# Kernel tuning notes

Hardware: AMD Instinct MI355X
Metric: run time of the kernel (lower is better)

The kernel has to match this reference:

```python
import jax, jax.numpy as jnp
import numpy as np

B, C, H, W = 4, 256, 64, 64
EPS = 1e-6


def setup_inputs() -> dict:
    key = jax.random.key(0)
    ks = jax.random.split(key, 6)
    x = jax.random.normal(ks[0], (B, C, H, W), jnp.float32)
    gn_w = jnp.ones((1, C, 1, 1), jnp.float32)
    gn_b = jnp.zeros((1, C, 1, 1), jnp.float32)
    s = 1.0 / np.sqrt(C)
    w0 = jax.random.normal(ks[1], (C, C), jnp.float32) * s
    w1 = jax.random.normal(ks[2], (C, C), jnp.float32) * s
    w2 = jax.random.normal(ks[3], (C, C), jnp.float32) * s
    w3 = jax.random.normal(ks[4], (C, C), jnp.float32) * s
    b0 = jnp.zeros((C,), jnp.float32)
    b1 = jnp.zeros((C,), jnp.float32)
    b2 = jnp.zeros((C,), jnp.float32)
    b3 = jnp.zeros((C,), jnp.float32)
    return {"x": x, "gn_w": gn_w, "gn_b": gn_b,
            "w0": w0, "b0": b0, "w1": w1, "b1": b1,
            "w2": w2, "b2": b2, "w3": w3, "b3": b3}


def _nin(t, Wm, bv):
    # 1x1 conv as channel matmul: (B,C,H,W) x (C,D) -> (B,D,H,W)
    return jnp.einsum('bchw,cd->bdhw', t, Wm) + bv[None, :, None, None]


def reference(x, gn_w, gn_b, w0, b0, w1, b1, w2, b2, w3, b3):
    Bb, Cc, Hh, Ww = x.shape
    G = min(Cc // 4, 32)  # GroupLayerNorm2d groups
    # per-pixel group norm: normalize over channels within each group only
    xg = x.reshape(Bb, G, Cc // G, Hh, Ww)
    mean = xg.mean(axis=2, keepdims=True)
    var = xg.var(axis=2, keepdims=True)
    hn = ((xg - mean) / jnp.sqrt(var + EPS)).reshape(Bb, Cc, Hh, Ww)
    hn = hn * gn_w + gn_b
    q = _nin(hn, w0, b0)
    k = _nin(hn, w1, b1)
    v = _nin(hn, w2, b2)
    # full (B,H,W,H,W) scores; mask is causal along W only (key col j > query col w)
    scores = jnp.einsum('bchw,bcij->bhwij', q, k) * (float(Cc) ** -0.5)
    causal = jnp.triu(jnp.ones((Ww, Ww), bool), k=1)  # (W_query, W_key)
    scores = jnp.where(causal[None, None, :, None, :], -jnp.inf, scores)
    attn = jax.nn.softmax(scores.reshape(Bb, Hh, Ww, Hh * Ww), axis=-1)
    attn = attn.reshape(Bb, Hh, Ww, Hh, Ww)
    h = jnp.einsum('bhwij,bcij->bchw', attn, v)
    return x + _nin(h, w3, b3)  # skip_rescale=False
```

## Files before the change

### kernel.cpp

```cpp
#include <hip/hip_runtime.h>
#include <math.h>

#define LOG2E 1.4426950408889634f

typedef __attribute__((ext_vector_type(8))) __bf16 bf16x8_t;
typedef __attribute__((ext_vector_type(8))) short short8_t;
typedef __attribute__((ext_vector_type(4))) short short4_t;
typedef __attribute__((ext_vector_type(4))) float f32x4;

static __device__ __forceinline__ short f2bf(float f){
    unsigned u = __builtin_bit_cast(unsigned, f);
    unsigned r = (u + 0x7fffu + ((u >> 16) & 1u)) >> 16;
    return (short)r;
}
static __device__ __forceinline__ float bf2f(short s){
    return __builtin_bit_cast(float, (unsigned)((unsigned short)s) << 16);
}

static __device__ __forceinline__ f32x4 mfma16(short8_t a, short8_t b, f32x4 c){
    return __builtin_amdgcn_mfma_f32_16x16x32_bf16(
        __builtin_bit_cast(bf16x8_t, a), __builtin_bit_cast(bf16x8_t, b), c, 0, 0, 0);
}

static __device__ __forceinline__ float swz16(float v){
    return __builtin_bit_cast(float,
        __builtin_amdgcn_ds_swizzle(__builtin_bit_cast(int, v), 0x401F));
}
static __device__ __forceinline__ float bperm32(int addr, float v){
    return __builtin_bit_cast(float,
        __builtin_amdgcn_ds_bpermute(addr, __builtin_bit_cast(int, v)));
}

static __device__ __forceinline__ void gload_lds16(const void* g, void* l){
    __builtin_amdgcn_global_load_lds(
        (const __attribute__((address_space(1))) unsigned char*)g,
        (__attribute__((address_space(3))) unsigned char*)l, 16, 0, 0);
}

__global__ __launch_bounds__(256) void prep_w(const float* __restrict__ w0,
    const float* __restrict__ w1, const float* __restrict__ w2,
    const float* __restrict__ w3, short* __restrict__ wT)
{
    __shared__ float T[64 * 65];
    const int mat = blockIdx.x >> 4, tile = blockIdx.x & 15;
    const int c0 = (tile >> 2) * 64, d0 = (tile & 3) * 64;
    const float* src = mat == 0 ? w0 : mat == 1 ? w1 : mat == 2 ? w2 : w3;
    const int t = threadIdx.x;
    #pragma unroll
    for (int i = 0; i < 4; i++){
        int r = (t >> 4) + i * 16, c4 = (t & 15) * 4;
        f32x4 v = *(const f32x4*)(src + (size_t)(c0 + r) * 256 + d0 + c4);
        #pragma unroll
        for (int j = 0; j < 4; j++) T[r * 65 + c4 + j] = v[j];
    }
    __syncthreads();
    int drow = t >> 2, cb = (t & 3) * 16;
    short tmp[16];
    #pragma unroll
    for (int j = 0; j < 16; j++) tmp[j] = f2bf(T[(cb + j) * 65 + drow]);
    short* dst = wT + (size_t)mat * 65536 + (size_t)(d0 + drow) * 256 + c0 + cb;
    *(short8_t*)dst = *(short8_t*)tmp;
    *(short8_t*)(dst + 8) = *(short8_t*)(tmp + 8);
}

__global__ __launch_bounds__(256) void gn_kernel(const float* __restrict__ x,
    const float* __restrict__ gnw, const float* __restrict__ gnb,
    short* __restrict__ hn)
{
    int flat = blockIdx.x * 256 + threadIdx.x;
    int n = flat & 4095, g = (flat >> 12) & 31, b = flat >> 17;
    const float* xp = x + (size_t)(b * 256 + g * 8) * 4096 + n;
    float v[8], s = 0.f, s2 = 0.f;
    #pragma unroll
    for (int k = 0; k < 8; k++){ float t = xp[(size_t)k * 4096]; v[k] = t; s += t; s2 += t * t; }
    float mean = s * 0.125f;
    float var  = s2 * 0.125f - mean * mean;
    float inv  = rsqrtf(var + 1e-6f);
    int h = n >> 6, w = n & 63, m = w * 64 + h;
    short o[8];
    #pragma unroll
    for (int k = 0; k < 8; k++)
        o[k] = f2bf((v[k] - mean) * inv * gnw[g * 8 + k] + gnb[g * 8 + k]);
    *(short8_t*)(hn + (size_t)(b * 4096 + m) * 256 + g * 8) = *(short8_t*)o;
}

__global__ __launch_bounds__(256) void qkv_gemm(const short* __restrict__ hn,
    const short* __restrict__ wT, const float* __restrict__ bq,
    const float* __restrict__ bk, const float* __restrict__ bv,
    short* __restrict__ Q, short* __restrict__ Kf, short* __restrict__ Vf)
{
    __shared__ short As[64 * 72];
    __shared__ short Bs[64 * 72];
    __shared__ float CT[64 * 65];

    const int tid = threadIdx.x;
    const int m0 = blockIdx.x * 64;
    const int by = blockIdx.y;
    const int mat = by >> 2;
    const int d0 = (by & 3) * 64;
    const short* w = wT + mat * 65536;
    const float* bias = mat == 0 ? bq : mat == 1 ? bk : bv;

    const int wv = tid >> 6, lane = tid & 63;
    const int wrow = (wv >> 1) * 32, wcol = (wv & 1) * 32;
    const int lrow = lane & 15, lq = lane >> 4;

    f32x4 acc[2][2] = {};

    for (int k0 = 0; k0 < 256; k0 += 64){
        __syncthreads();
        #pragma unroll
        for (int i = 0; i < 2; i++){
            int idx = tid + i * 256, r = idx >> 3, c = (idx & 7) * 8;
            *(short8_t*)&As[r * 72 + c] = *(const short8_t*)(hn + (size_t)(m0 + r) * 256 + k0 + c);
            *(short8_t*)&Bs[r * 72 + c] = *(const short8_t*)(w  + (size_t)(d0 + r) * 256 + k0 + c);
        }
        __syncthreads();
        #pragma unroll
        for (int kk = 0; kk < 2; kk++){
            int off = kk * 32 + lq * 8;
            short8_t a0  = *(short8_t*)&As[(wrow + lrow) * 72 + off];
            short8_t a1  = *(short8_t*)&As[(wrow + 16 + lrow) * 72 + off];
            short8_t b0v = *(short8_t*)&Bs[(wcol + lrow) * 72 + off];
            short8_t b1v = *(short8_t*)&Bs[(wcol + 16 + lrow) * 72 + off];
            acc[0][0] = mfma16(a0, b0v, acc[0][0]);
            acc[0][1] = mfma16(a0, b1v, acc[0][1]);
            acc[1][0] = mfma16(a1, b0v, acc[1][0]);
            acc[1][1] = mfma16(a1, b1v, acc[1][1]);
        }
    }

    const int b = m0 >> 12, kb64 = (m0 & 4095) >> 6;

    if (mat == 0){
        #pragma unroll
        for (int i = 0; i < 2; i++)
          #pragma unroll
          for (int j = 0; j < 2; j++)
            #pragma unroll
            for (int r = 0; r < 4; r++){
                int row = wrow + i * 16 + lq * 4 + r;
                int col = wcol + j * 16 + lrow;
                Q[(size_t)(m0 + row) * 256 + d0 + col] = f2bf((acc[i][j][r] + bias[d0 + col]) * 0.0625f);
            }
    } else if (mat == 1){
        #pragma unroll
        for (int i = 0; i < 2; i++)
          #pragma unroll
          for (int j = 0; j < 2; j++)
            #pragma unroll
            for (int r = 0; r < 4; r++){
                int row = wrow + i * 16 + lq * 4 + r;
                int col = wcol + j * 16 + lrow;
                CT[row * 65 + col] = acc[i][j][r] + bias[d0 + col];
            }
        __syncthreads();
        int key = tid >> 2, c16 = (tid & 3) * 16;
        int kc = key >> 4, l15 = key & 15;
        #pragma unroll
        for (int half = 0; half < 2; half++){
            int ch0 = c16 + half * 8;
            int ks = (d0 + ch0) >> 5, lqf = (ch0 & 31) >> 3;
            short tmp[8];
            #pragma unroll
            for (int j = 0; j < 8; j++) tmp[j] = f2bf(CT[key * 65 + ch0 + j]);
            size_t base = ((((size_t)(b * 64 + kb64)) * 4 + kc) * 8 + ks) * 512 + (lqf * 16 + l15) * 8;
            *(short8_t*)(Kf + base) = *(short8_t*)tmp;
        }
    } else {
        #pragma unroll
        for (int i = 0; i < 2; i++)
          #pragma unroll
          for (int j = 0; j < 2; j++)
            #pragma unroll
            for (int r = 0; r < 4; r++){
                int row = wrow + i * 16 + lq * 4 + r;
                int col = wcol + j * 16 + lrow;
                CT[col * 65 + row] = acc[i][j][r] + bias[d0 + col];
            }
        __syncthreads();
        const int kbd = kb64 >> 1, parity = kb64 & 1;
        const int cht_l = tid >> 6, lane_s = tid & 63;
        const int l15s = lane_s & 15, lg4s = lane_s >> 4;
        const int cht = (d0 >> 4) + cht_l;
        #pragma unroll
        for (int kc = 0; kc < 4; kc++){
            short tmp[4];
            #pragma unroll
            for (int j = 0; j < 4; j++)
                tmp[j] = f2bf(CT[(cht_l * 16 + l15s) * 65 + kc * 16 + lg4s * 4 + j]);
            size_t base = (size_t)b * 1048576 + (size_t)kbd * 32768 + kc * 8192
                        + cht * 512 + lane_s * 8 + parity * 4;
            *(short4_t*)(Vf + base) = *(short4_t*)tmp;
        }
    }
}

__global__ __launch_bounds__(256, 2) void attn_kernel(const short* __restrict__ Q,
    const short* __restrict__ Kf, const short* __restrict__ Vf,
    short* __restrict__ hb)
{
    __shared__ short SH[4 * 32 * 264];
    __shared__ float mls[4][32][2];

    const int tid = threadIdx.x, lane = tid & 63, kc = tid >> 6;
    const int l15 = lane & 15, lg4 = lane >> 4;
    const int a32 = ((lane ^ 32) << 2);

    const int id  = blockIdx.x;
    const int xcd = id & 7;
    const int b   = xcd >> 1;
    const int hh  = xcd & 1;
    const int r_  = id >> 3;
    const int t_  = r_ & 31;
    const int w   = (r_ & 32) ? 63 - t_ : t_;
    const int q0  = w * 64 + hh * 32;

    const short* Kb = Kf + (size_t)b * 1048576 + kc * 4096 + lane * 8;
    const short* Vg = Vf + (size_t)b * 1048576 + kc * 8192 + lane * 8;
    short* Vl = &SH[kc * 8192];

    short8_t qf0[8], qf1[8];
    {
        const short* qp0 = Q + ((size_t)b * 4096 + q0 + l15) * 256;
        const short* qp1 = qp0 + 16 * 256;
        #pragma unroll
        for (int ks = 0; ks < 8; ks++){
            qf0[ks] = *(const short8_t*)(qp0 + ks * 32 + lg4 * 8);
            qf1[ks] = *(const short8_t*)(qp1 + ks * 32 + lg4 * 8);
        }
    }

    f32x4 oacc0[16] = {}, oacc1[16] = {};
    float m0 = -1e30f, l0 = 0.f;
    float m1 = -1e30f, l1 = 0.f;

    short8_t kf[8];
    #pragma unroll
    for (int ks = 0; ks < 8; ks++) kf[ks] = *(const short8_t*)(Kb + ks * 512);

    for (int kb = 0; kb <= w; kb += 2){
        const bool has_odd = (kb + 1 <= w);

        f32x4 stA0 = {}, stA1 = {};
        #pragma unroll
        for (int ks = 0; ks < 8; ks++){
            stA0 = mfma16(kf[ks], qf0[ks], stA0);
            stA1 = mfma16(kf[ks], qf1[ks], stA1);
        }
        if (has_odd){
            const short* ka = Kb + (size_t)(kb + 1) * 16384;
            #pragma unroll
            for (int ks = 0; ks < 8; ks++) kf[ks] = *(const short8_t*)(ka + ks * 512);
        }
        {
            const short* vsrc = Vg + (size_t)(kb >> 1) * 32768;
            #pragma unroll
            for (int i = 0; i < 16; i++)
                gload_lds16(vsrc + i * 512, Vl + i * 512);
        }

        f32x4 pA0, pA1;
        {
            float tl0 = fmaxf(fmaxf(stA0[0], stA0[1]), fmaxf(stA0[2], stA0[3]));
            float tl1 = fmaxf(fmaxf(stA1[0], stA1[1]), fmaxf(stA1[2], stA1[3]));
            if (!__all(tl0 <= m0 + 5.f && tl1 <= m1 + 5.f)){
                float tm0 = fmaxf(tl0, swz16(tl0)); tm0 = fmaxf(tm0, bperm32(a32, tm0));
                float tm1 = fmaxf(tl1, swz16(tl1)); tm1 = fmaxf(tm1, bperm32(a32, tm1));
                float mn0 = fmaxf(m0, tm0), mn1 = fmaxf(m1, tm1);
                float al0 = exp2f((m0 - mn0) * LOG2E), al1 = exp2f((m1 - mn1) * LOG2E);
                l0 *= al0; l1 *= al1;
                #pragma unroll
                for (int i = 0; i < 16; i++){
                    #pragma unroll
                    for (int r = 0; r < 4; r++){ oacc0[i][r] *= al0; oacc1[i][r] *= al1; }
                }
                m0 = mn0; m1 = mn1;
            }
            #pragma unroll
            for (int r = 0; r < 4; r++){
                pA0[r] = exp2f((stA0[r] - m0) * LOG2E);
                pA1[r] = exp2f((stA1[r] - m1) * LOG2E);
            }
            l0 += (pA0[0] + pA0[1]) + (pA0[2] + pA0[3]);
            l1 += (pA1[0] + pA1[1]) + (pA1[2] + pA1[3]);
        }

        f32x4 pB0 = {0.f, 0.f, 0.f, 0.f}, pB1 = {0.f, 0.f, 0.f, 0.f};
        if (has_odd){
            f32x4 stB0 = {}, stB1 = {};
            #pragma unroll
            for (int ks = 0; ks < 8; ks++){
                stB0 = mfma16(kf[ks], qf0[ks], stB0);
                stB1 = mfma16(kf[ks], qf1[ks], stB1);
            }
            if (kb + 2 <= w){
                const short* ka = Kb + (size_t)(kb + 2) * 16384;
                #pragma unroll
                for (int ks = 0; ks < 8; ks++) kf[ks] = *(const short8_t*)(ka + ks * 512);
            }
            float tl0 = fmaxf(fmaxf(stB0[0], stB0[1]), fmaxf(stB0[2], stB0[3]));
            float tl1 = fmaxf(fmaxf(stB1[0], stB1[1]), fmaxf(stB1[2], stB1[3]));
            if (!__all(tl0 <= m0 + 5.f && tl1 <= m1 + 5.f)){
                float tm0 = fmaxf(tl0, swz16(tl0)); tm0 = fmaxf(tm0, bperm32(a32, tm0));
                float tm1 = fmaxf(tl1, swz16(tl1)); tm1 = fmaxf(tm1, bperm32(a32, tm1));
                float mn0 = fmaxf(m0, tm0), mn1 = fmaxf(m1, tm1);
                float al0 = exp2f((m0 - mn0) * LOG2E), al1 = exp2f((m1 - mn1) * LOG2E);
                l0 *= al0; l1 *= al1;
                #pragma unroll
                for (int i = 0; i < 16; i++){
                    #pragma unroll
                    for (int r = 0; r < 4; r++){ oacc0[i][r] *= al0; oacc1[i][r] *= al1; }
                }
                #pragma unroll
                for (int r = 0; r < 4; r++){ pA0[r] *= al0; pA1[r] *= al1; }
                m0 = mn0; m1 = mn1;
            }
            #pragma unroll
            for (int r = 0; r < 4; r++){
                pB0[r] = exp2f((stB0[r] - m0) * LOG2E);
                pB1[r] = exp2f((stB1[r] - m1) * LOG2E);
            }
            l0 += (pB0[0] + pB0[1]) + (pB0[2] + pB0[3]);
            l1 += (pB1[0] + pB1[1]) + (pB1[2] + pB1[3]);
        }

        short pk0[8], pk1[8];
        #pragma unroll
        for (int r = 0; r < 4; r++){
            pk0[r] = f2bf(pA0[r]); pk0[4 + r] = f2bf(pB0[r]);
            pk1[r] = f2bf(pA1[r]); pk1[4 + r] = f2bf(pB1[r]);
        }
        short8_t pbf0 = *(short8_t*)pk0;
        short8_t pbf1 = *(short8_t*)pk1;

        if (kb + 2 <= w){
            asm volatile("s_waitcnt vmcnt(8)" ::: "memory");
        } else {
            asm volatile("s_waitcnt vmcnt(0)" ::: "memory");
        }
        #pragma unroll
        for (int cht = 0; cht < 16; cht++){
            short8_t vfr = *(const short8_t*)(Vl + cht * 512 + lane * 8);
            oacc0[cht] = mfma16(vfr, pbf0, oacc0[cht]);
            oacc1[cht] = mfma16(vfr, pbf1, oacc1[cht]);
        }
    }

    float l0t = l0 + swz16(l0); l0t += bperm32(a32, l0t);
    float l1t = l1 + swz16(l1); l1t += bperm32(a32, l1t);

    if (lg4 == 0){
        mls[kc][l15][0] = m0;      mls[kc][l15][1] = l0t;
        mls[kc][16 + l15][0] = m1; mls[kc][16 + l15][1] = l1t;
    }
    __syncthreads();
    float sc0, sc1;
    {
        float ms0 = fmaxf(fmaxf(mls[0][l15][0], mls[1][l15][0]),
                          fmaxf(mls[2][l15][0], mls[3][l15][0]));
        float ms1 = fmaxf(fmaxf(mls[0][16 + l15][0], mls[1][16 + l15][0]),
                          fmaxf(mls[2][16 + l15][0], mls[3][16 + l15][0]));
        sc0 = exp2f((m0 - ms0) * LOG2E);
        sc1 = exp2f((m1 - ms1) * LOG2E);
    }
    #pragma unroll
    for (int cht = 0; cht < 16; cht++){
        short t4[4];
        #pragma unroll
        for (int r = 0; r < 4; r++) t4[r] = f2bf(oacc0[cht][r] * sc0);
        *(short4_t*)&SH[((kc * 32) + l15) * 264 + cht * 16 + lg4 * 4] = *(short4_t*)t4;
        #pragma unroll
        for (int r = 0; r < 4; r++) t4[r] = f2bf(oacc1[cht][r] * sc1);
        *(short4_t*)&SH[((kc * 32) + 16 + l15) * 264 + cht * 16 + lg4 * 4] = *(short4_t*)t4;
    }
    __syncthreads();
    {
        const int qq = tid & 31, cc = tid >> 5;
        float mv0 = mls[0][qq][0], mv1 = mls[1][qq][0], mv2 = mls[2][qq][0], mv3 = mls[3][qq][0];
        float ms = fmaxf(fmaxf(mv0, mv1), fmaxf(mv2, mv3));
        float Ls = mls[0][qq][1] * exp2f((mv0 - ms) * LOG2E)
                 + mls[1][qq][1] * exp2f((mv1 - ms) * LOG2E)
                 + mls[2][qq][1] * exp2f((mv2 - ms) * LOG2E)
                 + mls[3][qq][1] * exp2f((mv3 - ms) * LOG2E);
        float inv = 1.f / Ls;
        const int h = hh * 32 + qq;
        short* dst = hb + ((size_t)b * 4096 + h * 64 + w) * 256 + cc * 32;
        #pragma unroll
        for (int c8 = 0; c8 < 4; c8++){
            short8_t a0 = *(const short8_t*)&SH[((0 * 32) + qq) * 264 + cc * 32 + c8 * 8];
            short8_t a1 = *(const short8_t*)&SH[((1 * 32) + qq) * 264 + cc * 32 + c8 * 8];
            short8_t a2 = *(const short8_t*)&SH[((2 * 32) + qq) * 264 + cc * 32 + c8 * 8];
            short8_t a3 = *(const short8_t*)&SH[((3 * 32) + qq) * 264 + cc * 32 + c8 * 8];
            short t8[8];
            #pragma unroll
            for (int j = 0; j < 8; j++){
                float s = (bf2f(a0[j]) + bf2f(a1[j])) + (bf2f(a2[j]) + bf2f(a3[j]));
                t8[j] = f2bf(s * inv);
            }
            *(short8_t*)(dst + c8 * 8) = *(short8_t*)t8;
        }
    }
}

__global__ __launch_bounds__(256) void final_gemm(const short* __restrict__ hbuf,
    const short* __restrict__ wT3, const float* __restrict__ b3,
    const float* __restrict__ x, float* __restrict__ out)
{
    __shared__ short As[64 * 72];
    __shared__ short Bs[64 * 72];
    __shared__ float CT[64 * 65];

    const int tid = threadIdx.x;
    const int m0 = blockIdx.x * 64;
    const int d0 = blockIdx.y * 64;
    const int wv = tid >> 6, lane = tid & 63;
    const int wrow = (wv >> 1) * 32, wcol = (wv & 1) * 32;
    const int lrow = lane & 15, lq = lane >> 4;

    f32x4 acc[2][2] = {};
    for (int k0 = 0; k0 < 256; k0 += 64){
        __syncthreads();
        #pragma unroll
        for (int i = 0; i < 2; i++){
            int idx = tid + i * 256, r = idx >> 3, c = (idx & 7) * 8;
            *(short8_t*)&As[r * 72 + c] = *(const short8_t*)(hbuf + (size_t)(m0 + r) * 256 + k0 + c);
            *(short8_t*)&Bs[r * 72 + c] = *(const short8_t*)(wT3 + (size_t)(d0 + r) * 256 + k0 + c);
        }
        __syncthreads();
        #pragma unroll
        for (int kk = 0; kk < 2; kk++){
            int off = kk * 32 + lq * 8;
            short8_t a0  = *(short8_t*)&As[(wrow + lrow) * 72 + off];
            short8_t a1  = *(short8_t*)&As[(wrow + 16 + lrow) * 72 + off];
            short8_t b0v = *(short8_t*)&Bs[(wcol + lrow) * 72 + off];
            short8_t b1v = *(short8_t*)&Bs[(wcol + 16 + lrow) * 72 + off];
            acc[0][0] = mfma16(a0, b0v, acc[0][0]);
            acc[0][1] = mfma16(a0, b1v, acc[0][1]);
            acc[1][0] = mfma16(a1, b0v, acc[1][0]);
            acc[1][1] = mfma16(a1, b1v, acc[1][1]);
        }
    }
    #pragma unroll
    for (int i = 0; i < 2; i++)
      #pragma unroll
      for (int j = 0; j < 2; j++)
        #pragma unroll
        for (int r = 0; r < 4; r++){
            int row = wrow + i * 16 + lq * 4 + r;
            int col = wcol + j * 16 + lrow;
            CT[col * 65 + row] = acc[i][j][r] + b3[d0 + col];
        }
    __syncthreads();
    int b = m0 >> 12, n0 = m0 & 4095, hrow = n0 >> 6;
    int dr = tid >> 2, wc = (tid & 3) * 16;
    size_t base = ((size_t)(b * 256 + d0 + dr) * 64 + hrow) * 64 + wc;
    const f32x4* xp = (const f32x4*)(x + base);
    f32x4* op = (f32x4*)(out + base);
    #pragma unroll
    for (int q = 0; q < 4; q++){
        f32x4 xv = xp[q], o;
        #pragma unroll
        for (int j = 0; j < 4; j++) o[j] = xv[j] + CT[dr * 65 + wc + q * 4 + j];
        op[q] = o;
    }
}

extern "C" void kernel_launch(void* const* d_in, const int* in_sizes, int n_in,
                              void* d_out, int out_size, void* d_ws, size_t ws_size,
                              hipStream_t stream)
{
    const float* x   = (const float*)d_in[0];
    const float* gnw = (const float*)d_in[1];
    const float* gnb = (const float*)d_in[2];
    const float* w0  = (const float*)d_in[3];
    const float* b0  = (const float*)d_in[4];
    const float* w1  = (const float*)d_in[5];
    const float* b1  = (const float*)d_in[6];
    const float* w2  = (const float*)d_in[7];
    const float* b2  = (const float*)d_in[8];
    const float* w3  = (const float*)d_in[9];
    const float* b3  = (const float*)d_in[10];
    float* out = (float*)d_out;

    char* ws = (char*)d_ws;
    short* wT  = (short*)(ws);
    short* hn  = (short*)(ws + 524288);
    short* Qb  = (short*)(ws + 8912896);
    short* Kfb = (short*)(ws + 17301504);
    short* Vfb = (short*)(ws + 25690112);
    short* hb  = (short*)(ws + 34078720);

    prep_w   <<<64, 256, 0, stream>>>(w0, w1, w2, w3, wT);
    gn_kernel<<<2048, 256, 0, stream>>>(x, gnw, gnb, hn);
    qkv_gemm <<<dim3(256, 12), 256, 0, stream>>>(hn, wT, b0, b1, b2, Qb, Kfb, Vfb);
    attn_kernel<<<512, 256, 0, stream>>>(Qb, Kfb, Vfb, hb);
    final_gemm<<<dim3(256, 4), 256, 0, stream>>>(hb, wT + 3 * 65536, b3, x, out);
}
```

Before: 204.0 us.

## Pair complementary causal query columns per block and raise MFMA wave priority

Each attention block now has 512 threads and handles two query columns, w and 63-w, with four waves on each. Because the causal mask gives column w about w+1 key blocks, each block gets the same total work, and the grid shrinks from 512 to 256 blocks. The LDS layout is reorganised to give each wave its own V buffer, and the reduction scratch is split per column. s_setprio is raised around the MFMA loops so matrix-core waves get issue priority. The risks are lower occupancy from 128KB of LDS per block and only 256 blocks in flight, plus the shorter column's waves sitting idle at the shared barrier.

Result: no change. 208.0 us (+2.0%).

```diff
diff --git a/kernel.cpp b/kernel.cpp
--- a/kernel.cpp
+++ b/kernel.cpp
@@ -196,14 +196,15 @@
     }
 }
 
-__global__ __launch_bounds__(256, 2) void attn_kernel(const short* __restrict__ Q,
+__global__ __launch_bounds__(512, 2) void attn_kernel(const short* __restrict__ Q,
     const short* __restrict__ Kf, const short* __restrict__ Vf,
     short* __restrict__ hb)
 {
-    __shared__ short SH[4 * 32 * 264];
-    __shared__ float mls[4][32][2];
-
-    const int tid = threadIdx.x, lane = tid & 63, kc = tid >> 6;
+    __shared__ short SH[8 * 8192];
+    __shared__ float mls[2][4][32][2];
+
+    const int tid = threadIdx.x, lane = tid & 63, wv = tid >> 6;
+    const int kc = wv & 3, col = wv >> 2;
     const int l15 = lane & 15, lg4 = lane >> 4;
     const int a32 = ((lane ^ 32) << 2);
 
@@ -211,14 +212,13 @@
     const int xcd = id & 7;
     const int b   = xcd >> 1;
     const int hh  = xcd & 1;
-    const int r_  = id >> 3;
-    const int t_  = r_ & 31;
-    const int w   = (r_ & 32) ? 63 - t_ : t_;
+    const int w0  = id >> 3;
+    const int w   = col ? 63 - w0 : w0;
     const int q0  = w * 64 + hh * 32;
 
     const short* Kb = Kf + (size_t)b * 1048576 + kc * 4096 + lane * 8;
     const short* Vg = Vf + (size_t)b * 1048576 + kc * 8192 + lane * 8;
-    short* Vl = &SH[kc * 8192];
+    short* Vl = &SH[wv * 8192];
 
     short8_t qf0[8], qf1[8];
     {
@@ -243,11 +243,13 @@
         const bool has_odd = (kb + 1 <= w);
 
         f32x4 stA0 = {}, stA1 = {};
+        __builtin_amdgcn_s_setprio(1);
         #pragma unroll
         for (int ks = 0; ks < 8; ks++){
             stA0 = mfma16(kf[ks], qf0[ks], stA0);
             stA1 = mfma16(kf[ks], qf1[ks], stA1);
         }
+        __builtin_amdgcn_s_setprio(0);
         if (has_odd){
             const short* ka = Kb + (size_t)(kb + 1) * 16384;
             #pragma unroll
@@ -289,11 +291,13 @@
         f32x4 pB0 = {0.f, 0.f, 0.f, 0.f}, pB1 = {0.f, 0.f, 0.f, 0.f};
         if (has_odd){
             f32x4 stB0 = {}, stB1 = {};
+            __builtin_amdgcn_s_setprio(1);
             #pragma unroll
             for (int ks = 0; ks < 8; ks++){
                 stB0 = mfma16(kf[ks], qf0[ks], stB0);
                 stB1 = mfma16(kf[ks], qf1[ks], stB1);
             }
+            __builtin_amdgcn_s_setprio(0);
             if (kb + 2 <= w){
                 const short* ka = Kb + (size_t)(kb + 2) * 16384;
                 #pragma unroll
@@ -339,28 +343,30 @@
         } else {
             asm volatile("s_waitcnt vmcnt(0)" ::: "memory");
         }
+        __builtin_amdgcn_s_setprio(1);
         #pragma unroll
         for (int cht = 0; cht < 16; cht++){
             short8_t vfr = *(const short8_t*)(Vl + cht * 512 + lane * 8);
             oacc0[cht] = mfma16(vfr, pbf0, oacc0[cht]);
             oacc1[cht] = mfma16(vfr, pbf1, oacc1[cht]);
         }
+        __builtin_amdgcn_s_setprio(0);
     }
 
     float l0t = l0 + swz16(l0); l0t += bperm32(a32, l0t);
     float l1t = l1 + swz16(l1); l1t += bperm32(a32, l1t);
 
     if (lg4 == 0){
-        mls[kc][l15][0] = m0;      mls[kc][l15][1] = l0t;
-        mls[kc][16 + l15][0] = m1; mls[kc][16 + l15][1] = l1t;
+        mls[col][kc][l15][0] = m0;      mls[col][kc][l15][1] = l0t;
+        mls[col][kc][16 + l15][0] = m1; mls[col][kc][16 + l15][1] = l1t;
     }
     __syncthreads();
     float sc0, sc1;
     {
-        float ms0 = fmaxf(fmaxf(mls[0][l15][0], mls[1][l15][0]),
-                          fmaxf(mls[2][l15][0], mls[3][l15][0]));
-        float ms1 = fmaxf(fmaxf(mls[0][16 + l15][0], mls[1][16 + l15][0]),
-                          fmaxf(mls[2][16 + l15][0], mls[3][16 + l15][0]));
+        float ms0 = fmaxf(fmaxf(mls[col][0][l15][0], mls[col][1][l15][0]),
+                          fmaxf(mls[col][2][l15][0], mls[col][3][l15][0]));
+        float ms1 = fmaxf(fmaxf(mls[col][0][16 + l15][0], mls[col][1][16 + l15][0]),
+                          fmaxf(mls[col][2][16 + l15][0], mls[col][3][16 + l15][0]));
         sc0 = exp2f((m0 - ms0) * LOG2E);
         sc1 = exp2f((m1 - ms1) * LOG2E);
     }
@@ -369,29 +375,33 @@
         short t4[4];
         #pragma unroll
         for (int r = 0; r < 4; r++) t4[r] = f2bf(oacc0[cht][r] * sc0);
-        *(short4_t*)&SH[((kc * 32) + l15) * 264 + cht * 16 + lg4 * 4] = *(short4_t*)t4;
+        *(short4_t*)&SH[wv * 8192 + l15 * 256 + cht * 16 + lg4 * 4] = *(short4_t*)t4;
         #pragma unroll
         for (int r = 0; r < 4; r++) t4[r] = f2bf(oacc1[cht][r] * sc1);
-        *(short4_t*)&SH[((kc * 32) + 16 + l15) * 264 + cht * 16 + lg4 * 4] = *(short4_t*)t4;
+        *(short4_t*)&SH[wv * 8192 + (16 + l15) * 256 + cht * 16 + lg4 * 4] = *(short4_t*)t4;
     }
     __syncthreads();
     {
-        const int qq = tid & 31, cc = tid >> 5;
-        float mv0 = mls[0][qq][0], mv1 = mls[1][qq][0], mv2 = mls[2][qq][0], mv3 = mls[3][qq][0];
+        const int ccol = tid >> 8;
+        const int rem  = tid & 255;
+        const int qq   = rem & 31, cc = rem >> 5;
+        const int wc   = ccol ? 63 - w0 : w0;
+        float mv0 = mls[ccol][0][qq][0], mv1 = mls[ccol][1][qq][0];
+        float mv2 = mls[ccol][2][qq][0], mv3 = mls[ccol][3][qq][0];
         float ms = fmaxf(fmaxf(mv0, mv1), fmaxf(mv2, mv3));
-        float Ls = mls[0][qq][1] * exp2f((mv0 - ms) * LOG2E)
-                 + mls[1][qq][1] * exp2f((mv1 - ms) * LOG2E)
-                 + mls[2][qq][1] * exp2f((mv2 - ms) * LOG2E)
-                 + mls[3][qq][1] * exp2f((mv3 - ms) * LOG2E);
+        float Ls = mls[ccol][0][qq][1] * exp2f((mv0 - ms) * LOG2E)
+                 + mls[ccol][1][qq][1] * exp2f((mv1 - ms) * LOG2E)
+                 + mls[ccol][2][qq][1] * exp2f((mv2 - ms) * LOG2E)
+                 + mls[ccol][3][qq][1] * exp2f((mv3 - ms) * LOG2E);
         float inv = 1.f / Ls;
         const int h = hh * 32 + qq;
-        short* dst = hb + ((size_t)b * 4096 + h * 64 + w) * 256 + cc * 32;
+        short* dst = hb + ((size_t)b * 4096 + h * 64 + wc) * 256 + cc * 32;
         #pragma unroll
         for (int c8 = 0; c8 < 4; c8++){
-            short8_t a0 = *(const short8_t*)&SH[((0 * 32) + qq) * 264 + cc * 32 + c8 * 8];
-            short8_t a1 = *(const short8_t*)&SH[((1 * 32) + qq) * 264 + cc * 32 + c8 * 8];
-            short8_t a2 = *(const short8_t*)&SH[((2 * 32) + qq) * 264 + cc * 32 + c8 * 8];
-            short8_t a3 = *(const short8_t*)&SH[((3 * 32) + qq) * 264 + cc * 32 + c8 * 8];
+            short8_t a0 = *(const short8_t*)&SH[(ccol * 4 + 0) * 8192 + qq * 256 + cc * 32 + c8 * 8];
+            short8_t a1 = *(const short8_t*)&SH[(ccol * 4 + 1) * 8192 + qq * 256 + cc * 32 + c8 * 8];
+            short8_t a2 = *(const short8_t*)&SH[(ccol * 4 + 2) * 8192 + qq * 256 + cc * 32 + c8 * 8];
+            short8_t a3 = *(const short8_t*)&SH[(ccol * 4 + 3) * 8192 + qq * 256 + cc * 32 + c8 * 8];
             short t8[8];
             #pragma unroll
             for (int j = 0; j < 8; j++){
@@ -494,6 +504,6 @@
     prep_w   <<<64, 256, 0, stream>>>(w0, w1, w2, w3, wT);
     gn_kernel<<<2048, 256, 0, stream>>>(x, gnw, gnb, hn);
     qkv_gemm <<<dim3(256, 12), 256, 0, stream>>>(hn, wT, b0, b1, b2, Qb, Kfb, Vfb);
-    attn_kernel<<<512, 256, 0, stream>>>(Qb, Kfb, Vfb, hb);
+    attn_kernel<<<256, 512, 0, stream>>>(Qb, Kfb, Vfb, hb);
     final_gemm<<<dim3(256, 4), 256, 0, stream>>>(hb, wT + 3 * 65536, b3, x, out);
 }
```

## Widen QKV and output GEMM tiles to full 256 output channels per block

Applied to the files above, without the earlier changes.

Both GEMM kernels now compute a 64x256 output tile per block instead of 64x64, so each block loads its A tile once and reuses it across all output channels. Grid sizes drop accordingly (256x3 and 256 blocks). The epilogue is staged through shared memory in four 64-channel chunks with extra barriers. The trade-off is more registers (16 accumulators per wave), a larger shared-memory B tile, and fewer blocks, which may reduce occupancy and parallelism on a large GPU.

Measured after the change: 209.9 us. 2.9% more time.

```diff
diff --git a/kernel.cpp b/kernel.cpp
--- a/kernel.cpp
+++ b/kernel.cpp
@@ -84,28 +84,26 @@
     *(short8_t*)(hn + (size_t)(b * 4096 + m) * 256 + g * 8) = *(short8_t*)o;
 }
 
-__global__ __launch_bounds__(256) void qkv_gemm(const short* __restrict__ hn,
+__global__ __launch_bounds__(256, 2) void qkv_gemm(const short* __restrict__ hn,
     const short* __restrict__ wT, const float* __restrict__ bq,
     const float* __restrict__ bk, const float* __restrict__ bv,
     short* __restrict__ Q, short* __restrict__ Kf, short* __restrict__ Vf)
 {
     __shared__ short As[64 * 72];
-    __shared__ short Bs[64 * 72];
+    __shared__ short Bs[256 * 72];
     __shared__ float CT[64 * 65];
 
     const int tid = threadIdx.x;
     const int m0 = blockIdx.x * 64;
-    const int by = blockIdx.y;
-    const int mat = by >> 2;
-    const int d0 = (by & 3) * 64;
+    const int mat = blockIdx.y;
     const short* w = wT + mat * 65536;
     const float* bias = mat == 0 ? bq : mat == 1 ? bk : bv;
 
     const int wv = tid >> 6, lane = tid & 63;
-    const int wrow = (wv >> 1) * 32, wcol = (wv & 1) * 32;
+    const int wrow = (wv >> 1) * 32, wcol = (wv & 1) * 128;
     const int lrow = lane & 15, lq = lane >> 4;
 
-    f32x4 acc[2][2] = {};
+    f32x4 acc[2][8] = {};
 
     for (int k0 = 0; k0 < 256; k0 += 64){
         __syncthreads();
@@ -113,20 +111,24 @@
         for (int i = 0; i < 2; i++){
             int idx = tid + i * 256, r = idx >> 3, c = (idx & 7) * 8;
             *(short8_t*)&As[r * 72 + c] = *(const short8_t*)(hn + (size_t)(m0 + r) * 256 + k0 + c);
-            *(short8_t*)&Bs[r * 72 + c] = *(const short8_t*)(w  + (size_t)(d0 + r) * 256 + k0 + c);
+        }
+        #pragma unroll
+        for (int i = 0; i < 8; i++){
+            int idx = tid + i * 256, r = idx >> 3, c = (idx & 7) * 8;
+            *(short8_t*)&Bs[r * 72 + c] = *(const short8_t*)(w + (size_t)r * 256 + k0 + c);
         }
         __syncthreads();
         #pragma unroll
         for (int kk = 0; kk < 2; kk++){
             int off = kk * 32 + lq * 8;
-            short8_t a0  = *(short8_t*)&As[(wrow + lrow) * 72 + off];
-            short8_t a1  = *(short8_t*)&As[(wrow + 16 + lrow) * 72 + off];
-            short8_t b0v = *(short8_t*)&Bs[(wcol + lrow) * 72 + off];
-            short8_t b1v = *(short8_t*)&Bs[(wcol + 16 + lrow) * 72 + off];
-            acc[0][0] = mfma16(a0, b0v, acc[0][0]);
-            acc[0][1] = mfma16(a0, b1v, acc[0][1]);
-            acc[1][0] = mfma16(a1, b0v, acc[1][0]);
-            acc[1][1] = mfma16(a1, b1v, acc[1][1]);
+            short8_t a0 = *(short8_t*)&As[(wrow + lrow) * 72 + off];
+            short8_t a1 = *(short8_t*)&As[(wrow + 16 + lrow) * 72 + off];
+            #pragma unroll
+            for (int j = 0; j < 8; j++){
+                short8_t b8 = *(short8_t*)&Bs[(wcol + j * 16 + lrow) * 72 + off];
+                acc[0][j] = mfma16(a0, b8, acc[0][j]);
+                acc[1][j] = mfma16(a1, b8, acc[1][j]);
+            }
         }
     }
 
@@ -136,62 +138,77 @@
         #pragma unroll
         for (int i = 0; i < 2; i++)
           #pragma unroll
-          for (int j = 0; j < 2; j++)
+          for (int j = 0; j < 8; j++)
             #pragma unroll
             for (int r = 0; r < 4; r++){
                 int row = wrow + i * 16 + lq * 4 + r;
                 int col = wcol + j * 16 + lrow;
-                Q[(size_t)(m0 + row) * 256 + d0 + col] = f2bf((acc[i][j][r] + bias[d0 + col]) * 0.0625f);
+                Q[(size_t)(m0 + row) * 256 + col] = f2bf((acc[i][j][r] + bias[col]) * 0.0625f);
             }
     } else if (mat == 1){
         #pragma unroll
-        for (int i = 0; i < 2; i++)
-          #pragma unroll
-          for (int j = 0; j < 2; j++)
-            #pragma unroll
-            for (int r = 0; r < 4; r++){
-                int row = wrow + i * 16 + lq * 4 + r;
-                int col = wcol + j * 16 + lrow;
-                CT[row * 65 + col] = acc[i][j][r] + bias[d0 + col];
-            }
-        __syncthreads();
-        int key = tid >> 2, c16 = (tid & 3) * 16;
-        int kc = key >> 4, l15 = key & 15;
-        #pragma unroll
-        for (int half = 0; half < 2; half++){
-            int ch0 = c16 + half * 8;
-            int ks = (d0 + ch0) >> 5, lqf = (ch0 & 31) >> 3;
-            short tmp[8];
-            #pragma unroll
-            for (int j = 0; j < 8; j++) tmp[j] = f2bf(CT[key * 65 + ch0 + j]);
-            size_t base = ((((size_t)(b * 64 + kb64)) * 4 + kc) * 8 + ks) * 512 + (lqf * 16 + l15) * 8;
-            *(short8_t*)(Kf + base) = *(short8_t*)tmp;
+        for (int d0c = 0; d0c < 4; d0c++){
+            __syncthreads();
+            if ((wv & 1) == (d0c >> 1)){
+                int jb = (d0c & 1) * 4;
+                #pragma unroll
+                for (int i = 0; i < 2; i++)
+                  #pragma unroll
+                  for (int jj = 0; jj < 4; jj++)
+                    #pragma unroll
+                    for (int r = 0; r < 4; r++){
+                        int row = wrow + i * 16 + lq * 4 + r;
+                        int colL = jj * 16 + lrow;
+                        CT[row * 65 + colL] = acc[i][jb + jj][r] + bias[d0c * 64 + colL];
+                    }
+            }
+            __syncthreads();
+            int key = tid >> 2, c16 = (tid & 3) * 16;
+            int kc = key >> 4, l15 = key & 15;
+            int d0 = d0c * 64;
+            #pragma unroll
+            for (int half = 0; half < 2; half++){
+                int ch0 = c16 + half * 8;
+                int ks = (d0 + ch0) >> 5, lqf = (ch0 & 31) >> 3;
+                short tmp[8];
+                #pragma unroll
+                for (int j = 0; j < 8; j++) tmp[j] = f2bf(CT[key * 65 + ch0 + j]);
+                size_t base = ((((size_t)(b * 64 + kb64)) * 4 + kc) * 8 + ks) * 512 + (lqf * 16 + l15) * 8;
+                *(short8_t*)(Kf + base) = *(short8_t*)tmp;
+            }
         }
     } else {
-        #pragma unroll
-        for (int i = 0; i < 2; i++)
-          #pragma unroll
-          for (int j = 0; j < 2; j++)
-            #pragma unroll
-            for (int r = 0; r < 4; r++){
-                int row = wrow + i * 16 + lq * 4 + r;
-                int col = wcol + j * 16 + lrow;
-                CT[col * 65 + row] = acc[i][j][r] + bias[d0 + col];
-            }
-        __syncthreads();
         const int kbd = kb64 >> 1, parity = kb64 & 1;
-        const int cht_l = tid >> 6, lane_s = tid & 63;
-        const int l15s = lane_s & 15, lg4s = lane_s >> 4;
-        const int cht = (d0 >> 4) + cht_l;
-        #pragma unroll
-        for (int kc = 0; kc < 4; kc++){
-            short tmp[4];
-            #pragma unroll
-            for (int j = 0; j < 4; j++)
-                tmp[j] = f2bf(CT[(cht_l * 16 + l15s) * 65 + kc * 16 + lg4s * 4 + j]);
-            size_t base = (size_t)b * 1048576 + (size_t)kbd * 32768 + kc * 8192
-                        + cht * 512 + lane_s * 8 + parity * 4;
-            *(short4_t*)(Vf + base) = *(short4_t*)tmp;
+        #pragma unroll
+        for (int d0c = 0; d0c < 4; d0c++){
+            __syncthreads();
+            if ((wv & 1) == (d0c >> 1)){
+                int jb = (d0c & 1) * 4;
+                #pragma unroll
+                for (int i = 0; i < 2; i++)
+                  #pragma unroll
+                  for (int jj = 0; jj < 4; jj++)
+                    #pragma unroll
+                    for (int r = 0; r < 4; r++){
+                        int row = wrow + i * 16 + lq * 4 + r;
+                        int colL = jj * 16 + lrow;
+                        CT[colL * 65 + row] = acc[i][jb + jj][r] + bias[d0c * 64 + colL];
+                    }
+            }
+            __syncthreads();
+            const int cht_l = tid >> 6, lane_s = tid & 63;
+            const int l15s = lane_s & 15, lg4s = lane_s >> 4;
+            const int cht = d0c * 4 + cht_l;
+            #pragma unroll
+            for (int kc = 0; kc < 4; kc++){
+                short tmp[4];
+                #pragma unroll
+                for (int j = 0; j < 4; j++)
+                    tmp[j] = f2bf(CT[(cht_l * 16 + l15s) * 65 + kc * 16 + lg4s * 4 + j]);
+                size_t base = (size_t)b * 1048576 + (size_t)kbd * 32768 + kc * 8192
+                            + cht * 512 + lane_s * 8 + parity * 4;
+                *(short4_t*)(Vf + base) = *(short4_t*)tmp;
+            }
         }
     }
 }
@@ -403,66 +420,77 @@
     }
 }
 
-__global__ __launch_bounds__(256) void final_gemm(const short* __restrict__ hbuf,
+__global__ __launch_bounds__(256, 2) void final_gemm(const short* __restrict__ hbuf,
     const short* __restrict__ wT3, const float* __restrict__ b3,
     const float* __restrict__ x, float* __restrict__ out)
 {
     __shared__ short As[64 * 72];
-    __shared__ short Bs[64 * 72];
+    __shared__ short Bs[256 * 72];
     __shared__ float CT[64 * 65];
 
     const int tid = threadIdx.x;
     const int m0 = blockIdx.x * 64;
-    const int d0 = blockIdx.y * 64;
     const int wv = tid >> 6, lane = tid & 63;
-    const int wrow = (wv >> 1) * 32, wcol = (wv & 1) * 32;
+    const int wrow = (wv >> 1) * 32, wcol = (wv & 1) * 128;
     const int lrow = lane & 15, lq = lane >> 4;
 
-    f32x4 acc[2][2] = {};
+    f32x4 acc[2][8] = {};
     for (int k0 = 0; k0 < 256; k0 += 64){
         __syncthreads();
         #pragma unroll
         for (int i = 0; i < 2; i++){
             int idx = tid + i * 256, r = idx >> 3, c = (idx & 7) * 8;
             *(short8_t*)&As[r * 72 + c] = *(const short8_t*)(hbuf + (size_t)(m0 + r) * 256 + k0 + c);
-            *(short8_t*)&Bs[r * 72 + c] = *(const short8_t*)(wT3 + (size_t)(d0 + r) * 256 + k0 + c);
+        }
+        #pragma unroll
+        for (int i = 0; i < 8; i++){
+            int idx = tid + i * 256, r = idx >> 3, c = (idx & 7) * 8;
+            *(short8_t*)&Bs[r * 72 + c] = *(const short8_t*)(wT3 + (size_t)r * 256 + k0 + c);
         }
         __syncthreads();
         #pragma unroll
         for (int kk = 0; kk < 2; kk++){
             int off = kk * 32 + lq * 8;
-            short8_t a0  = *(short8_t*)&As[(wrow + lrow) * 72 + off];
-            short8_t a1  = *(short8_t*)&As[(wrow + 16 + lrow) * 72 + off];
-            short8_t b0v = *(short8_t*)&Bs[(wcol + lrow) * 72 + off];
-            short8_t b1v = *(short8_t*)&Bs[(wcol + 16 + lrow) * 72 + off];
-            acc[0][0] = mfma16(a0, b0v, acc[0][0]);
-            acc[0][1] = mfma16(a0, b1v, acc[0][1]);
-            acc[1][0] = mfma16(a1, b0v, acc[1][0]);
-            acc[1][1] = mfma16(a1, b1v, acc[1][1]);
-        }
-    }
-    #pragma unroll
-    for (int i = 0; i < 2; i++)
-      #pragma unroll
-      for (int j = 0; j < 2; j++)
-        #pragma unroll
-        for (int r = 0; r < 4; r++){
-            int row = wrow + i * 16 + lq * 4 + r;
-            int col = wcol + j * 16 + lrow;
-            CT[col * 65 + row] = acc[i][j][r] + b3[d0 + col];
-        }
-    __syncthreads();
-    int b = m0 >> 12, n0 = m0 & 4095, hrow = n0 >> 6;
-    int dr = tid >> 2, wc = (tid & 3) * 16;
-    size_t base = ((size_t)(b * 256 + d0 + dr) * 64 + hrow) * 64 + wc;
-    const f32x4* xp = (const f32x4*)(x + base);
-    f32x4* op = (f32x4*)(out + base);
-    #pragma unroll
-    for (int q = 0; q < 4; q++){
-        f32x4 xv = xp[q], o;
-        #pragma unroll
-        for (int j = 0; j < 4; j++) o[j] = xv[j] + CT[dr * 65 + wc + q * 4 + j];
-        op[q] = o;
+            short8_t a0 = *(short8_t*)&As[(wrow + lrow) * 72 + off];
+            short8_t a1 = *(short8_t*)&As[(wrow + 16 + lrow) * 72 + off];
+            #pragma unroll
+            for (int j = 0; j < 8; j++){
+                short8_t b8 = *(short8_t*)&Bs[(wcol + j * 16 + lrow) * 72 + off];
+                acc[0][j] = mfma16(a0, b8, acc[0][j]);
+                acc[1][j] = mfma16(a1, b8, acc[1][j]);
+            }
+        }
+    }
+
+    const int b = m0 >> 12, n0 = m0 & 4095, hrow = n0 >> 6;
+    #pragma unroll
+    for (int d0c = 0; d0c < 4; d0c++){
+        __syncthreads();
+        if ((wv & 1) == (d0c >> 1)){
+            int jb = (d0c & 1) * 4;
+            #pragma unroll
+            for (int i = 0; i < 2; i++)
+              #pragma unroll
+              for (int jj = 0; jj < 4; jj++)
+                #pragma unroll
+                for (int r = 0; r < 4; r++){
+                    int row = wrow + i * 16 + lq * 4 + r;
+                    int colL = jj * 16 + lrow;
+                    CT[colL * 65 + row] = acc[i][jb + jj][r] + b3[d0c * 64 + colL];
+                }
+        }
+        __syncthreads();
+        int dr = tid >> 2, wc = (tid & 3) * 16;
+        size_t base = ((size_t)(b * 256 + d0c * 64 + dr) * 64 + hrow) * 64 + wc;
+        const f32x4* xp = (const f32x4*)(x + base);
+        f32x4* op = (f32x4*)(out + base);
+        #pragma unroll
+        for (int q = 0; q < 4; q++){
+            f32x4 xv = xp[q], o;
+            #pragma unroll
+            for (int j = 0; j < 4; j++) o[j] = xv[j] + CT[dr * 65 + wc + q * 4 + j];
+            op[q] = o;
+        }
     }
 }
 
@@ -493,7 +521,7 @@
 
     prep_w   <<<64, 256, 0, stream>>>(w0, w1, w2, w3, wT);
     gn_kernel<<<2048, 256, 0, stream>>>(x, gnw, gnb, hn);
-    qkv_gemm <<<dim3(256, 12), 256, 0, stream>>>(hn, wT, b0, b1, b2, Qb, Kfb, Vfb);
+    qkv_gemm <<<dim3(256, 3), 256, 0, stream>>>(hn, wT, b0, b1, b2, Qb, Kfb, Vfb);
     attn_kernel<<<512, 256, 0, stream>>>(Qb, Kfb, Vfb, hb);
-    final_gemm<<<dim3(256, 4), 256, 0, stream>>>(hb, wT + 3 * 65536, b3, x, out);
-}
+    final_gemm<<<256, 256, 0, stream>>>(hb, wT + 3 * 65536, b3, x, out);
+}
```
